# Performance work log

Hardware: AMD Instinct MI355X
Metric: run time of the kernel (lower is better)

Reference implementation:

```python
import jax, jax.numpy as jnp
import numpy as np

# Static config (matches init_kwargs)
B, H, W, C = 8, 80, 60, 512
WS, SHIFT = 10, 5
NH = 16
HD = C // NH  # 32
L = WS * WS  # 100 tokens per window
NW = (H // WS) * (W // WS)  # 48 windows per image
EPS = 1e-5


def _relative_position_index():
    coords = np.stack(np.meshgrid(np.arange(WS), np.arange(WS), indexing='ij'))  # (2,WS,WS)
    flat = coords.reshape(2, -1)  # (2, L)
    rel = flat[:, :, None] - flat[:, None, :]  # (2, L, L)
    rel = rel.transpose(1, 2, 0)  # (L, L, 2)
    rel[:, :, 0] += WS - 1
    rel[:, :, 1] += WS - 1
    rel[:, :, 0] *= 2 * WS - 1
    return rel.sum(-1)  # (L, L) indices into (2*WS-1)^2 table


def _attn_mask():
    # Swin shift mask: label 3x3 regions, tokens in different regions cannot attend.
    img = np.zeros((H, W), dtype=np.float32)
    slices = (slice(0, -WS), slice(-WS, -SHIFT), slice(-SHIFT, None))
    cnt = 0
    for hs in slices:
        for ws_ in slices:
            img[hs, ws_] = cnt
            cnt += 1
    mw = img.reshape(H // WS, WS, W // WS, WS).transpose(0, 2, 1, 3).reshape(NW, L)
    diff = mw[:, None, :] - mw[:, :, None]  # (NW, L, L)
    return np.where(diff != 0, -100.0, 0.0).astype(np.float32)


REL_IDX = jnp.asarray(_relative_position_index())
ATTN_MASK = jnp.asarray(_attn_mask())


def layernorm(x, g, b):
    mu = jnp.mean(x, axis=-1, keepdims=True)
    var = jnp.mean(jnp.square(x - mu), axis=-1, keepdims=True)
    return (x - mu) * jax.lax.rsqrt(var + EPS) * g + b


def setup_inputs() -> dict:
    key = jax.random.key(0)
    ks = jax.random.split(key, 8)
    s = 0.02
    return {
        'hidden_states': jax.random.normal(ks[0], (B, H * W, C), jnp.float32),
        'ln1_g': jnp.ones((C,), jnp.float32),
        'ln1_b': jnp.zeros((C,), jnp.float32),
        'wq': jax.random.normal(ks[1], (C, C), jnp.float32) * s,
        'bq': jnp.zeros((C,), jnp.float32),
        'wk': jax.random.normal(ks[2], (C, C), jnp.float32) * s,
        'bk': jnp.zeros((C,), jnp.float32),
        'wv': jax.random.normal(ks[3], (C, C), jnp.float32) * s,
        'bv': jnp.zeros((C,), jnp.float32),
        'wo': jax.random.normal(ks[4], (C, C), jnp.float32) * s,
        'bo': jnp.zeros((C,), jnp.float32),
        'rel_bias_table': jax.random.normal(ks[5], ((2 * WS - 1) ** 2, NH), jnp.float32) * s,
        'ln2_g': jnp.ones((C,), jnp.float32),
        'ln2_b': jnp.zeros((C,), jnp.float32),
        'w1': jax.random.normal(ks[6], (C, 4 * C), jnp.float32) * s,
        'b1': jnp.zeros((4 * C,), jnp.float32),
        'w2': jax.random.normal(ks[7], (4 * C, C), jnp.float32) * s,
        'b2': jnp.zeros((C,), jnp.float32),
    }


def reference(hidden_states, ln1_g, ln1_b, wq, bq, wk, bk, wv, bv, wo, bo,
              rel_bias_table, ln2_g, ln2_b, w1, b1, w2, b2):
    shortcut = hidden_states  # (B, H*W, C)
    x = layernorm(hidden_states, ln1_g, ln1_b).reshape(B, H, W, C)
    # cyclic shift (H, W divisible by WS -> no padding needed)
    x = jnp.roll(x, (-SHIFT, -SHIFT), axis=(1, 2))
    # window partition -> (B*NW, L, C)
    win = x.reshape(B, H // WS, WS, W // WS, WS, C).transpose(0, 1, 3, 2, 4, 5)
    win = win.reshape(B * NW, L, C)
    # multi-head attention within windows
    q = (win @ wq + bq).reshape(-1, L, NH, HD).transpose(0, 2, 1, 3)
    k = (win @ wk + bk).reshape(-1, L, NH, HD).transpose(0, 2, 1, 3)
    v = (win @ wv + bv).reshape(-1, L, NH, HD).transpose(0, 2, 1, 3)
    scores = jnp.einsum('bhqd,bhkd->bhqk', q, k) / np.sqrt(HD).astype(np.float32)
    bias = rel_bias_table[REL_IDX.reshape(-1)].reshape(L, L, NH).transpose(2, 0, 1)
    scores = scores + bias[None]  # (B*NW, NH, L, L)
    scores = scores.reshape(B, NW, NH, L, L) + ATTN_MASK[None, :, None]
    attn = jax.nn.softmax(scores.reshape(B * NW, NH, L, L), axis=-1)
    ctx = jnp.einsum('bhqk,bhkd->bhqd', attn, v).transpose(0, 2, 1, 3).reshape(B * NW, L, C)
    out = ctx @ wo + bo
    # window reverse + un-shift
    out = out.reshape(B, H // WS, W // WS, WS, WS, C).transpose(0, 1, 3, 2, 4, 5)
    out = out.reshape(B, H, W, C)
    out = jnp.roll(out, (SHIFT, SHIFT), axis=(1, 2)).reshape(B, H * W, C)
    hs = shortcut + out
    # FFN with post-residual layernorm input
    y = layernorm(hs, ln2_g, ln2_b)
    y = jax.nn.gelu(y @ w1 + b1, approximate=False) @ w2 + b2
    return hs + y
```

## Files before the change

kernel.cpp:

```cpp
#include <hip/hip_runtime.h>
#include <math.h>

typedef unsigned short u16;
typedef unsigned int u32;
typedef __bf16 bf16x8 __attribute__((ext_vector_type(8)));
typedef float f32x4 __attribute__((ext_vector_type(4)));

__device__ __forceinline__ float b2f(u16 u) { return __uint_as_float(((u32)u) << 16); }
__device__ __forceinline__ u16 f2b(float f) {
    u32 x = __float_as_uint(f);
    return (u16)((x + 0x7FFFu + ((x >> 16) & 1u)) >> 16);
}
__device__ __forceinline__ void load8f(const float* p, size_t idx, float* o) {
    const float4* q = (const float4*)(p + idx);
    float4 a = q[0], b = q[1];
    o[0]=a.x; o[1]=a.y; o[2]=a.z; o[3]=a.w; o[4]=b.x; o[5]=b.y; o[6]=b.z; o[7]=b.w;
}
__device__ __forceinline__ void gld16(const void* g, void* l) {
    __builtin_amdgcn_global_load_lds(
        (const __attribute__((address_space(1))) u32*)g,
        (__attribute__((address_space(3))) u32*)l, 16, 0, 0);
}

__global__ __launch_bounds__(256) void transpose_k(const float* __restrict__ Win, u16* __restrict__ Wt,
                                                   int Kd, int Nd, float scale) {
    __shared__ u16 tile[32][33];
    int tx = threadIdx.x & 31, ty = threadIdx.x >> 5;
    int k0 = blockIdx.x << 5, n0 = blockIdx.y << 5;
#pragma unroll
    for (int r = 0; r < 4; r++)
        tile[ty + 8 * r][tx] = f2b(Win[(size_t)(k0 + ty + 8 * r) * Nd + (n0 + tx)] * scale);
    __syncthreads();
#pragma unroll
    for (int r = 0; r < 4; r++)
        Wt[(size_t)(n0 + ty + 8 * r) * Kd + (k0 + tx)] = tile[tx][ty + 8 * r];
}

__global__ __launch_bounds__(256) void biascat_k(const float* __restrict__ bq, const float* __restrict__ bk,
                                                 const float* __restrict__ bv, float* __restrict__ o) {
    int i = blockIdx.x * 256 + threadIdx.x;
    float v = (i < 512) ? bq[i] * 0.17677669529663689f : (i < 1024 ? bk[i - 512] : bv[i - 1024]);
    o[i] = v;
}

__global__ __launch_bounds__(256) void ln1win_k(const float* __restrict__ x, const float* __restrict__ g,
                                                const float* __restrict__ bta, u16* __restrict__ win) {
    int wave = threadIdx.x >> 6, lane = threadIdx.x & 63;
    int token = blockIdx.x * 4 + wave;
    int b = token / 4800, rem = token - b * 4800;
    int h = rem / 60, w = rem - h * 60;
    int hr = h + 75; if (hr >= 80) hr -= 80;
    int wr = w + 55; if (wr >= 60) wr -= 60;
    int widx = (hr / 10) * 6 + (wr / 10);
    int l = (hr - (hr / 10) * 10) * 10 + (wr - (wr / 10) * 10);
    size_t dstrow = ((size_t)b * 48 + widx) * 100 + l;
    int c0 = lane * 8;
    float v[8]; load8f(x, (size_t)token * 512 + c0, v);
    float s = 0.f, s2 = 0.f;
#pragma unroll
    for (int e = 0; e < 8; e++) { s += v[e]; s2 += v[e] * v[e]; }
#pragma unroll
    for (int o = 32; o > 0; o >>= 1) { s += __shfl_xor(s, o); s2 += __shfl_xor(s2, o); }
    float mean = s * (1.0f / 512.0f);
    float var = fmaxf(s2 * (1.0f / 512.0f) - mean * mean, 0.0f);
    float rstd = rsqrtf(var + 1e-5f);
    uint4 o4; u16* ou = (u16*)&o4;
#pragma unroll
    for (int e = 0; e < 8; e++)
        ou[e] = f2b((v[e] - mean) * rstd * g[c0 + e] + bta[c0 + e]);
    *(uint4*)(win + dstrow * 512 + c0) = o4;
}

__global__ __launch_bounds__(256) void resid2_k(const float* __restrict__ shortcut, const u16* __restrict__ attn_out,
                                                const float* __restrict__ g, const float* __restrict__ bta,
                                                u16* __restrict__ hs, u16* __restrict__ ln2y) {
    int wave = threadIdx.x >> 6, lane = threadIdx.x & 63;
    int token = blockIdx.x * 4 + wave;
    int b = token / 4800, rem = token - b * 4800;
    int h = rem / 60, w = rem - h * 60;
    int hr = h + 75; if (hr >= 80) hr -= 80;
    int wr = w + 55; if (wr >= 60) wr -= 60;
    int widx = (hr / 10) * 6 + (wr / 10);
    int l = (hr - (hr / 10) * 10) * 10 + (wr - (wr / 10) * 10);
    size_t arow = ((size_t)b * 48 + widx) * 100 + l;
    int c0 = lane * 8;
    float sv[8]; load8f(shortcut, (size_t)token * 512 + c0, sv);
    uint4 da = *(const uint4*)(attn_out + arow * 512 + c0);
    const u16* au = (const u16*)&da;
    float hv[8]; float s = 0.f, s2 = 0.f;
    uint4 oh; u16* ohu = (u16*)&oh;
#pragma unroll
    for (int e = 0; e < 8; e++) {
        hv[e] = sv[e] + b2f(au[e]);
        s += hv[e]; s2 += hv[e] * hv[e];
        ohu[e] = f2b(hv[e]);
    }
    *(uint4*)(hs + (size_t)token * 512 + c0) = oh;
#pragma unroll
    for (int off = 32; off > 0; off >>= 1) { s += __shfl_xor(s, off); s2 += __shfl_xor(s2, off); }
    float mean = s * (1.0f / 512.0f);
    float var = fmaxf(s2 * (1.0f / 512.0f) - mean * mean, 0.0f);
    float rstd = rsqrtf(var + 1e-5f);
    uint4 oy; u16* oyu = (u16*)&oy;
#pragma unroll
    for (int e = 0; e < 8; e++)
        oyu[e] = f2b((hv[e] - mean) * rstd * g[c0 + e] + bta[c0 + e]);
    *(uint4*)(ln2y + (size_t)token * 512 + c0) = oy;
}

template <int EPI, int OF32, int QKV>
__global__ __launch_bounds__(256) void gemm_k(const u16* __restrict__ A, const u16* __restrict__ Bt,
                                              const float* __restrict__ bias, const u16* __restrict__ res,
                                              void* __restrict__ C0, void* __restrict__ C1, void* __restrict__ C2,
                                              int M, int N, int K) {
    __shared__ __align__(16) u16 As[3][128 * 32];
    __shared__ __align__(16) u16 Bs[3][128 * 32];
    int tid = threadIdx.x;
    int wave = tid >> 6, lane = tid & 63;
    int l15 = lane & 15, quad = lane >> 4;
    int lq = lane >> 2, lr = lane & 3;
    int wm = (wave >> 1) * 64, wn = (wave & 1) * 64;

    int gy = gridDim.y;
    int nwg = gridDim.x * gy;
    int lid = blockIdx.x + blockIdx.y * gridDim.x;
    int xcd = lid & 7, loc = lid >> 3;
    int q8 = nwg >> 3, r8 = nwg & 7;
    int wg = (xcd < r8 ? xcd * (q8 + 1) : r8 * (q8 + 1) + (xcd - r8) * q8) + loc;
    int bn = wg % gy, bm = wg / gy;

    f32x4 acc[4][4];
#pragma unroll
    for (int i = 0; i < 4; i++)
#pragma unroll
        for (int j = 0; j < 4; j++) acc[i][j] = (f32x4){0.f, 0.f, 0.f, 0.f};

    const u16* Ab = A + (size_t)(bm * 128) * K;
    const u16* Bb = Bt + (size_t)(bn * 128) * K;

    int T = K >> 5;
    auto STAGE = [&](int b, int t) {
        int kt = t << 5;
#pragma unroll
        for (int h = 0; h < 2; h++) {
            int r = h * 64 + wave * 16 + lq;
            gld16(Ab + (size_t)r * K + kt + lr * 8, &As[b][(h * 64 + wave * 16) * 32]);
            gld16(Bb + (size_t)r * K + kt + lr * 8, &Bs[b][(h * 64 + wave * 16) * 32]);
        }
    };

    STAGE(0, 0);
    STAGE(1, 1);
    for (int t = 0; t < T; t++) {
        int cb = t % 3;
        if (t + 2 < T) STAGE((t + 2) % 3, t + 2);
        if (t + 2 < T)      asm volatile("s_waitcnt vmcnt(8)" ::: "memory");
        else if (t + 1 < T) asm volatile("s_waitcnt vmcnt(4)" ::: "memory");
        else                asm volatile("s_waitcnt vmcnt(0)" ::: "memory");
        __builtin_amdgcn_s_barrier();
        asm volatile("" ::: "memory");
        bf16x8 af[4], bfr[4];
#pragma unroll
        for (int x = 0; x < 4; x++) {
            af[x]  = *(const bf16x8*)(&As[cb][(wm + x * 16 + l15) * 32 + quad * 8]);
            bfr[x] = *(const bf16x8*)(&Bs[cb][(wn + x * 16 + l15) * 32 + quad * 8]);
        }
        asm volatile("s_waitcnt lgkmcnt(0)" ::: "memory");
        __builtin_amdgcn_sched_barrier(0);
        __builtin_amdgcn_s_barrier();
        asm volatile("" ::: "memory");
#pragma unroll
        for (int i = 0; i < 4; i++)
#pragma unroll
            for (int j = 0; j < 4; j++)
                acc[i][j] = __builtin_amdgcn_mfma_f32_16x16x32_bf16(af[i], bfr[j], acc[i][j], 0, 0, 0);
    }

    u16* Cd = (u16*)C0;
    if (QKV) {
        int sel = bn >> 2;
        Cd = (sel == 0) ? (u16*)C0 : (sel == 1) ? (u16*)C1 : (u16*)C2;
    }
#pragma unroll
    for (int i = 0; i < 4; i++) {
        int row0 = bm * 128 + wm + i * 16 + quad * 4;
#pragma unroll
        for (int j = 0; j < 4; j++) {
            int colg = bn * 128 + wn + j * 16 + l15;
            int col = QKV ? (colg & 511) : colg;
            float bv = bias[colg];
#pragma unroll
            for (int rr = 0; rr < 4; rr++) {
                int row = row0 + rr;
                float v = acc[i][j][rr] + bv;
                if (EPI == 1) {
                    float zz = 1.5957691216f * (v + 0.044715f * v * v * v);
                    float t = 1.0f - 2.0f / (__expf(zz) + 1.0f);
                    v = 0.5f * v * (1.0f + t);
                }
                if (EPI == 2) v += b2f(res[(size_t)row * 512 + col]);
                if (OF32) ((float*)Cd)[(size_t)row * N + col] = v;
                else      ((u16*)Cd)[(size_t)row * N + col] = f2b(v);
            }
        }
    }
}

__global__ __launch_bounds__(256) void biasprep_k(const float* __restrict__ table, u16* __restrict__ biasM) {
    int idx = blockIdx.x * 256 + threadIdx.x;
    int k = idx % 112;
    int t = idx / 112;
    int q = t % 100; t /= 100;
    int head = t & 15, wt = t >> 4;
    float v;
    if (k >= 100) {
        v = -1e30f;
    } else {
        int qi = q / 10, qj = q - qi * 10;
        int ki = k / 10, kj = k - ki * 10;
        int rel = (qi - ki) * 19 + (qj - kj) + 180;
        v = table[rel * 16 + head];
        int rq = ((wt & 2) ? (qi < 5 ? 4 : 8) : 0) + ((wt & 1) ? (qj < 5 ? 1 : 2) : 0);
        int rk = ((wt & 2) ? (ki < 5 ? 4 : 8) : 0) + ((wt & 1) ? (kj < 5 ? 1 : 2) : 0);
        if (rq != rk) v -= 100.0f;
    }
    biasM[idx] = f2b(v);
}

__global__ __launch_bounds__(256, 3) void attn_mfma_k(const u16* __restrict__ Q, const u16* __restrict__ Km,
                                                      const u16* __restrict__ V, const u16* __restrict__ biasM,
                                                      u16* __restrict__ ctx) {
    __shared__ __align__(16) u16 lds[4 * 6144];
    int tid = threadIdx.x;
    int wave = tid >> 6, lane = tid & 63;
    int l15 = lane & 15, quad = lane >> 4;
    int bid = blockIdx.x;
    int win = bid >> 2;
    int head = ((bid & 3) << 2) + wave;
    int w48 = win % 48;
    int wh = w48 / 6, ww = w48 - wh * 6;
    int wtype = ((wh == 7) ? 2 : 0) + ((ww == 5) ? 1 : 0);
    size_t base = (size_t)win * 51200 + head * 32;
    u16* Vt = lds + wave * 6144;
    u16* Pl = Vt + 4096;
    const u16* bptr = biasM + (size_t)(wtype * 16 + head) * 11200;

    {
        uint4 z = {0u, 0u, 0u, 0u};
#pragma unroll
        for (int r = 0; r < 2; r++) {
            int c = r * 64 + lane;
            int d = c >> 2, seg = c & 3;
            int k0 = 96 + seg * 8;
            *(uint4*)(Vt + d * 128 + (k0 ^ ((d & 7) << 3))) = z;
        }
        uint2 z2 = {0u, 0u};
        *(uint2*)(Pl + l15 * 128 + ((112 + quad * 4) ^ ((l15 & 7) << 3))) = z2;
    }
#pragma unroll
    for (int r = 0; r < 2; r++) {
        int k = r * 64 + lane;
        if (k < 100) {
            const uint4* vp = (const uint4*)(V + base + (size_t)k * 512);
#pragma unroll
            for (int c = 0; c < 4; c++) {
                uint4 dv = vp[c];
                const u16* e = (const u16*)&dv;
#pragma unroll
                for (int t = 0; t < 8; t++) {
                    int d = c * 8 + t;
                    Vt[d * 128 + (k ^ ((d & 7) << 3))] = e[t];
                }
            }
        }
    }
    bf16x8 kf[7];
#pragma unroll
    for (int i = 0; i < 7; i++) {
        int kr = i * 16 + l15; if (kr > 99) kr = 99;
        kf[i] = *(const bf16x8*)(Km + base + (size_t)kr * 512 + quad * 8);
    }
    bf16x8 vf[2][4];
#pragma unroll
    for (int it = 0; it < 2; it++)
#pragma unroll
        for (int ks = 0; ks < 4; ks++) {
            int D = it * 16 + l15;
            vf[it][ks] = *(const bf16x8*)(Vt + D * 128 + ((ks * 32 + quad * 8) ^ ((D & 7) << 3)));
        }

#pragma unroll 1
    for (int j = 0; j < 7; j++) {
        int q = j * 16 + l15;
        int qc = q > 99 ? 99 : q;
        bf16x8 qf = *(const bf16x8*)(Q + base + (size_t)qc * 512 + quad * 8);
        f32x4 s[7];
#pragma unroll
        for (int i = 0; i < 7; i++) {
            uint2 bb = *(const uint2*)(bptr + (size_t)qc * 112 + i * 16 + quad * 4);
            const u16* be = (const u16*)&bb;
            s[i][0] = b2f(be[0]); s[i][1] = b2f(be[1]);
            s[i][2] = b2f(be[2]); s[i][3] = b2f(be[3]);
        }
#pragma unroll
        for (int i = 0; i < 7; i++)
            s[i] = __builtin_amdgcn_mfma_f32_16x16x32_bf16(kf[i], qf, s[i], 0, 0, 0);
        float m = -1e30f;
#pragma unroll
        for (int i = 0; i < 7; i++)
#pragma unroll
            for (int rr = 0; rr < 4; rr++) m = fmaxf(m, s[i][rr]);
        m = fmaxf(m, __shfl_xor(m, 16));
        m = fmaxf(m, __shfl_xor(m, 32));
        float l = 0.f;
#pragma unroll
        for (int i = 0; i < 7; i++)
#pragma unroll
            for (int rr = 0; rr < 4; rr++) { s[i][rr] = __expf(s[i][rr] - m); l += s[i][rr]; }
        l += __shfl_xor(l, 16);
        l += __shfl_xor(l, 32);
#pragma unroll
        for (int i = 0; i < 7; i++) {
            u32 lo, hi;
            asm("v_cvt_pk_bf16_f32 %0, %1, %2" : "=v"(lo) : "v"(s[i][0]), "v"(s[i][1]));
            asm("v_cvt_pk_bf16_f32 %0, %1, %2" : "=v"(hi) : "v"(s[i][2]), "v"(s[i][3]));
            uint2 w; w.x = lo; w.y = hi;
            *(uint2*)(Pl + l15 * 128 + ((i * 16 + quad * 4) ^ ((l15 & 7) << 3))) = w;
        }
        f32x4 o0 = (f32x4){0.f, 0.f, 0.f, 0.f};
        f32x4 o1 = (f32x4){0.f, 0.f, 0.f, 0.f};
#pragma unroll
        for (int ks = 0; ks < 4; ks++) {
            bf16x8 pf = *(const bf16x8*)(Pl + l15 * 128 + ((ks * 32 + quad * 8) ^ ((l15 & 7) << 3)));
            o0 = __builtin_amdgcn_mfma_f32_16x16x32_bf16(vf[0][ks], pf, o0, 0, 0, 0);
            o1 = __builtin_amdgcn_mfma_f32_16x16x32_bf16(vf[1][ks], pf, o1, 0, 0, 0);
        }
        float inv = 1.0f / l;
        if (q < 100) {
            u16* cp = ctx + base + (size_t)q * 512;
            {
                float a0 = o0[0]*inv, a1 = o0[1]*inv, a2 = o0[2]*inv, a3 = o0[3]*inv;
                u32 lo, hi;
                asm("v_cvt_pk_bf16_f32 %0, %1, %2" : "=v"(lo) : "v"(a0), "v"(a1));
                asm("v_cvt_pk_bf16_f32 %0, %1, %2" : "=v"(hi) : "v"(a2), "v"(a3));
                uint2 w; w.x = lo; w.y = hi;
                *(uint2*)(cp + quad * 4) = w;
            }
            {
                float a0 = o1[0]*inv, a1 = o1[1]*inv, a2 = o1[2]*inv, a3 = o1[3]*inv;
                u32 lo, hi;
                asm("v_cvt_pk_bf16_f32 %0, %1, %2" : "=v"(lo) : "v"(a0), "v"(a1));
                asm("v_cvt_pk_bf16_f32 %0, %1, %2" : "=v"(hi) : "v"(a2), "v"(a3));
                uint2 w; w.x = lo; w.y = hi;
                *(uint2*)(cp + 16 + quad * 4) = w;
            }
        }
    }
}

extern "C" void kernel_launch(void* const* d_in, const int* in_sizes, int n_in,
                              void* d_out, int out_size, void* d_ws, size_t ws_size,
                              hipStream_t stream) {
    const float* hidden = (const float*)d_in[0];
    const float* ln1_g  = (const float*)d_in[1];
    const float* ln1_b  = (const float*)d_in[2];
    const float* wq = (const float*)d_in[3];  const float* bq = (const float*)d_in[4];
    const float* wk = (const float*)d_in[5];  const float* bk = (const float*)d_in[6];
    const float* wv = (const float*)d_in[7];  const float* bv = (const float*)d_in[8];
    const float* wo = (const float*)d_in[9];  const float* bo = (const float*)d_in[10];
    const float* rel = (const float*)d_in[11];
    const float* ln2_g = (const float*)d_in[12];
    const float* ln2_b = (const float*)d_in[13];
    const float* w1 = (const float*)d_in[14]; const float* b1 = (const float*)d_in[15];
    const float* w2 = (const float*)d_in[16]; const float* b2 = (const float*)d_in[17];

    const size_t NTC = 38400ull * 512;
    u16* ws = (u16*)d_ws;
    u16* R0 = ws;
    u16* R1 = ws + NTC;
    u16* Rh = ws + 2 * NTC;
    u16* wqt = ws + 3 * NTC;
    u16* wkt = wqt + 512 * 512;
    u16* wvt = wkt + 512 * 512;
    u16* wot = wvt + 512 * 512;
    u16* w1t = wot + 512 * 512;
    u16* w2t = w1t + 1048576;
    float* qkvb = (float*)(w2t + 1048576);
    u16* dlo = (u16*)d_out;
    u16* biasM = dlo + NTC;
    float* outp = (float*)d_out;

    const float SC = 0.17677669529663689f;

    transpose_k<<<dim3(16, 16), 256, 0, stream>>>(wq, wqt, 512, 512, SC);
    transpose_k<<<dim3(16, 16), 256, 0, stream>>>(wk, wkt, 512, 512, 1.0f);
    transpose_k<<<dim3(16, 16), 256, 0, stream>>>(wv, wvt, 512, 512, 1.0f);
    transpose_k<<<dim3(16, 16), 256, 0, stream>>>(wo, wot, 512, 512, 1.0f);
    transpose_k<<<dim3(16, 64), 256, 0, stream>>>(w1, w1t, 512, 2048, 1.0f);
    transpose_k<<<dim3(64, 16), 256, 0, stream>>>(w2, w2t, 2048, 512, 1.0f);
    biascat_k<<<6, 256, 0, stream>>>(bq, bk, bv, qkvb);
    biasprep_k<<<2800, 256, 0, stream>>>(rel, biasM);

    ln1win_k<<<9600, 256, 0, stream>>>(hidden, ln1_g, ln1_b, R0 );

    gemm_k<0, 0, 1><<<dim3(300, 12), 256, 0, stream>>>(R0, wqt, qkvb, nullptr,
                                                       R1 , Rh , dlo , 38400, 512, 512);

    attn_mfma_k<<<1536, 256, 0, stream>>>(R1, Rh, dlo, biasM, R0 );

    gemm_k<0, 0, 0><<<dim3(300, 4), 256, 0, stream>>>(R0, wot, bo, nullptr,
                                                      R1 , nullptr, nullptr, 38400, 512, 512);

    resid2_k<<<9600, 256, 0, stream>>>(hidden, R1, ln2_g, ln2_b, Rh , dlo );

    for (int mc = 1; mc >= 0; mc--) {
        size_t roff = (size_t)mc * 19200 * 512;
        gemm_k<1, 0, 0><<<dim3(150, 16), 256, 0, stream>>>(dlo + roff, w1t, b1, nullptr,
                                                           R0 , nullptr, nullptr, 19200, 2048, 512);
        gemm_k<2, 1, 0><<<dim3(150, 4), 256, 0, stream>>>(R0, w2t, b2, Rh + roff,
                                                          outp + roff, nullptr, nullptr, 19200, 512, 2048);
    }
}
```

Before: 724.9 us.

## Enlarge GEMM tiles to 256x256x64 with 8 waves, swizzled LDS and split-phase prefetch

Rewrites the bf16 MFMA GEMM to use 256x256 output tiles with K-step 64, 512 threads (8 waves, each computing 128x64), and double-buffered LDS with an XOR swizzle to avoid bank conflicts. Global-to-LDS prefetch of the next tile is interleaved between MFMA phases, and s_setprio raises priority around the MFMA bursts. The aim is higher arithmetic intensity per LDS/global byte and better latency hiding. In exchange it uses more registers and LDS (128 KB) and launches a quarter as many workgroups, which can hurt occupancy or tail balance on the 38400x512 GEMMs.

Result: slower. 752.3 us (+3.8%).

```diff
diff --git a/kernel.cpp b/kernel.cpp
--- a/kernel.cpp
+++ b/kernel.cpp
@@ -109,17 +109,16 @@
 }
 
 template <int EPI, int OF32, int QKV>
-__global__ __launch_bounds__(256) void gemm_k(const u16* __restrict__ A, const u16* __restrict__ Bt,
-                                              const float* __restrict__ bias, const u16* __restrict__ res,
-                                              void* __restrict__ C0, void* __restrict__ C1, void* __restrict__ C2,
-                                              int M, int N, int K) {
-    __shared__ __align__(16) u16 As[3][128 * 32];
-    __shared__ __align__(16) u16 Bs[3][128 * 32];
+__global__ __launch_bounds__(512, 2) void gemm_k(const u16* __restrict__ A, const u16* __restrict__ Bt,
+                                                 const float* __restrict__ bias, const u16* __restrict__ res,
+                                                 void* __restrict__ C0, void* __restrict__ C1, void* __restrict__ C2,
+                                                 int M, int N, int K) {
+    __shared__ __align__(16) u16 As[2][256 * 64];
+    __shared__ __align__(16) u16 Bs[2][256 * 64];
     int tid = threadIdx.x;
     int wave = tid >> 6, lane = tid & 63;
     int l15 = lane & 15, quad = lane >> 4;
-    int lq = lane >> 2, lr = lane & 3;
-    int wm = (wave >> 1) * 64, wn = (wave & 1) * 64;
+    int wr = wave >> 2, wc = wave & 3;
 
     int gy = gridDim.y;
     int nwg = gridDim.x * gy;
@@ -129,74 +128,115 @@
     int wg = (xcd < r8 ? xcd * (q8 + 1) : r8 * (q8 + 1) + (xcd - r8) * q8) + loc;
     int bn = wg % gy, bm = wg / gy;
 
-    f32x4 acc[4][4];
-#pragma unroll
-    for (int i = 0; i < 4; i++)
+    f32x4 acc[8][4];
+#pragma unroll
+    for (int i = 0; i < 8; i++)
 #pragma unroll
         for (int j = 0; j < 4; j++) acc[i][j] = (f32x4){0.f, 0.f, 0.f, 0.f};
 
-    const u16* Ab = A + (size_t)(bm * 128) * K;
-    const u16* Bb = Bt + (size_t)(bn * 128) * K;
-
-    int T = K >> 5;
-    auto STAGE = [&](int b, int t) {
-        int kt = t << 5;
-#pragma unroll
-        for (int h = 0; h < 2; h++) {
-            int r = h * 64 + wave * 16 + lq;
-            gld16(Ab + (size_t)r * K + kt + lr * 8, &As[b][(h * 64 + wave * 16) * 32]);
-            gld16(Bb + (size_t)r * K + kt + lr * 8, &Bs[b][(h * 64 + wave * 16) * 32]);
-        }
+    const u16* Ab = A + (size_t)(bm * 256) * K;
+    const u16* Bb = Bt + (size_t)(bn * 256) * K;
+
+    int lrow = lane >> 3;
+    int cg = (lane & 7) ^ lrow;
+    size_t gOff = (size_t)(wave * 8 + lrow) * K + cg * 8;
+    int e = l15 & 7;
+    int xk0 = (quad ^ e) * 8;
+    int xk1 = xk0 ^ 32;
+    int aRow = (wr * 128 + l15) * 64;
+    int bRow = (wc * 64 + l15) * 64;
+
+    auto STAGE_A = [&](int b, int kt, int i) {
+        gld16(Ab + (size_t)(i * 64) * K + kt + gOff, &As[b][(i * 64 + wave * 8) * 64]);
     };
-
-    STAGE(0, 0);
-    STAGE(1, 1);
+    auto STAGE_B = [&](int b, int kt, int j) {
+        gld16(Bb + (size_t)(j * 64) * K + kt + gOff, &Bs[b][(j * 64 + wave * 8) * 64]);
+    };
+
+#define MM16(MH)                                                                     \
+    do {                                                                             \
+        __builtin_amdgcn_s_setprio(1);                                               \
+        _Pragma("unroll") for (int i_ = 0; i_ < 4; i_++)                             \
+            _Pragma("unroll") for (int n_ = 0; n_ < 4; n_++)                         \
+                acc[(MH) * 4 + i_][n_] = __builtin_amdgcn_mfma_f32_16x16x32_bf16(    \
+                    a_[i_], b_[n_], acc[(MH) * 4 + i_][n_], 0, 0, 0);                \
+        __builtin_amdgcn_s_setprio(0);                                               \
+    } while (0)
+
+    int T = K >> 6;
+    STAGE_B(0, 0, 0); STAGE_B(0, 0, 1);
+    STAGE_B(0, 0, 2); STAGE_B(0, 0, 3);
+    STAGE_A(0, 0, 0); STAGE_A(0, 0, 2);
+    STAGE_A(0, 0, 1); STAGE_A(0, 0, 3);
+
+#pragma unroll 1
     for (int t = 0; t < T; t++) {
-        int cb = t % 3;
-        if (t + 2 < T) STAGE((t + 2) % 3, t + 2);
-        if (t + 2 < T)      asm volatile("s_waitcnt vmcnt(8)" ::: "memory");
-        else if (t + 1 < T) asm volatile("s_waitcnt vmcnt(4)" ::: "memory");
-        else                asm volatile("s_waitcnt vmcnt(0)" ::: "memory");
+        int cur = t & 1, nxt = cur ^ 1;
+        int ktn = (t + 1) << 6;
+        bool pf = (t + 1 < T);
+        bf16x8 a_[4], b_[4];
+        if (pf) {
+            STAGE_B(nxt, ktn, 0); STAGE_B(nxt, ktn, 1);
+            asm volatile("s_waitcnt vmcnt(4)" ::: "memory");
+        } else {
+            asm volatile("s_waitcnt vmcnt(2)" ::: "memory");
+        }
         __builtin_amdgcn_s_barrier();
         asm volatile("" ::: "memory");
-        bf16x8 af[4], bfr[4];
-#pragma unroll
-        for (int x = 0; x < 4; x++) {
-            af[x]  = *(const bf16x8*)(&As[cb][(wm + x * 16 + l15) * 32 + quad * 8]);
-            bfr[x] = *(const bf16x8*)(&Bs[cb][(wn + x * 16 + l15) * 32 + quad * 8]);
-        }
+#pragma unroll
+        for (int n = 0; n < 4; n++) b_[n] = *(const bf16x8*)(&Bs[cur][bRow + n * 1024 + xk0]);
+#pragma unroll
+        for (int i = 0; i < 4; i++) a_[i] = *(const bf16x8*)(&As[cur][aRow + i * 1024 + xk0]);
+        MM16(0);
+        if (pf) {
+            STAGE_B(nxt, ktn, 2); STAGE_B(nxt, ktn, 3);
+            asm volatile("s_waitcnt vmcnt(4)" ::: "memory");
+        } else {
+            asm volatile("s_waitcnt vmcnt(0)" ::: "memory");
+        }
+        __builtin_amdgcn_s_barrier();
+        asm volatile("" ::: "memory");
+#pragma unroll
+        for (int i = 0; i < 4; i++) a_[i] = *(const bf16x8*)(&As[cur][aRow + (4 + i) * 1024 + xk0]);
+        MM16(1);
+        if (pf) { STAGE_A(nxt, ktn, 0); STAGE_A(nxt, ktn, 2); }
+#pragma unroll
+        for (int n = 0; n < 4; n++) b_[n] = *(const bf16x8*)(&Bs[cur][bRow + n * 1024 + xk1]);
+#pragma unroll
+        for (int i = 0; i < 4; i++) a_[i] = *(const bf16x8*)(&As[cur][aRow + i * 1024 + xk1]);
+        MM16(0);
+        if (pf) { STAGE_A(nxt, ktn, 1); STAGE_A(nxt, ktn, 3); }
+#pragma unroll
+        for (int i = 0; i < 4; i++) a_[i] = *(const bf16x8*)(&As[cur][aRow + (4 + i) * 1024 + xk1]);
         asm volatile("s_waitcnt lgkmcnt(0)" ::: "memory");
         __builtin_amdgcn_sched_barrier(0);
         __builtin_amdgcn_s_barrier();
         asm volatile("" ::: "memory");
-#pragma unroll
-        for (int i = 0; i < 4; i++)
-#pragma unroll
-            for (int j = 0; j < 4; j++)
-                acc[i][j] = __builtin_amdgcn_mfma_f32_16x16x32_bf16(af[i], bfr[j], acc[i][j], 0, 0, 0);
-    }
+        MM16(1);
+    }
+#undef MM16
 
     u16* Cd = (u16*)C0;
     if (QKV) {
-        int sel = bn >> 2;
+        int sel = bn >> 1;
         Cd = (sel == 0) ? (u16*)C0 : (sel == 1) ? (u16*)C1 : (u16*)C2;
     }
 #pragma unroll
-    for (int i = 0; i < 4; i++) {
-        int row0 = bm * 128 + wm + i * 16 + quad * 4;
-#pragma unroll
-        for (int j = 0; j < 4; j++) {
-            int colg = bn * 128 + wn + j * 16 + l15;
+    for (int m = 0; m < 8; m++) {
+        int row0 = bm * 256 + wr * 128 + m * 16 + quad * 4;
+#pragma unroll
+        for (int n = 0; n < 4; n++) {
+            int colg = bn * 256 + wc * 64 + n * 16 + l15;
             int col = QKV ? (colg & 511) : colg;
             float bv = bias[colg];
 #pragma unroll
             for (int rr = 0; rr < 4; rr++) {
                 int row = row0 + rr;
-                float v = acc[i][j][rr] + bv;
+                float v = acc[m][n][rr] + bv;
                 if (EPI == 1) {
                     float zz = 1.5957691216f * (v + 0.044715f * v * v * v);
-                    float t = 1.0f - 2.0f / (__expf(zz) + 1.0f);
-                    v = 0.5f * v * (1.0f + t);
+                    float tt = 1.0f - 2.0f / (__expf(zz) + 1.0f);
+                    v = 0.5f * v * (1.0f + tt);
                 }
                 if (EPI == 2) v += b2f(res[(size_t)row * 512 + col]);
                 if (OF32) ((float*)Cd)[(size_t)row * N + col] = v;
@@ -403,21 +443,21 @@
 
     ln1win_k<<<9600, 256, 0, stream>>>(hidden, ln1_g, ln1_b, R0 );
 
-    gemm_k<0, 0, 1><<<dim3(300, 12), 256, 0, stream>>>(R0, wqt, qkvb, nullptr,
-                                                       R1 , Rh , dlo , 38400, 512, 512);
+    gemm_k<0, 0, 1><<<dim3(150, 6), 512, 0, stream>>>(R0, wqt, qkvb, nullptr,
+                                                      R1 , Rh , dlo , 38400, 512, 512);
 
     attn_mfma_k<<<1536, 256, 0, stream>>>(R1, Rh, dlo, biasM, R0 );
 
-    gemm_k<0, 0, 0><<<dim3(300, 4), 256, 0, stream>>>(R0, wot, bo, nullptr,
+    gemm_k<0, 0, 0><<<dim3(150, 2), 512, 0, stream>>>(R0, wot, bo, nullptr,
                                                       R1 , nullptr, nullptr, 38400, 512, 512);
 
     resid2_k<<<9600, 256, 0, stream>>>(hidden, R1, ln2_g, ln2_b, Rh , dlo );
 
     for (int mc = 1; mc >= 0; mc--) {
         size_t roff = (size_t)mc * 19200 * 512;
-        gemm_k<1, 0, 0><<<dim3(150, 16), 256, 0, stream>>>(dlo + roff, w1t, b1, nullptr,
-                                                           R0 , nullptr, nullptr, 19200, 2048, 512);
-        gemm_k<2, 1, 0><<<dim3(150, 4), 256, 0, stream>>>(R0, w2t, b2, Rh + roff,
-                                                          outp + roff, nullptr, nullptr, 19200, 512, 2048);
-    }
-}
+        gemm_k<1, 0, 0><<<dim3(75, 8), 512, 0, stream>>>(dlo + roff, w1t, b1, nullptr,
+                                                         R0 , nullptr, nullptr, 19200, 2048, 512);
+        gemm_k<2, 1, 0><<<dim3(75, 2), 512, 0, stream>>>(R0, w2t, b2, Rh + roff,
+                                                         outp + roff, nullptr, nullptr, 19200, 512, 2048);
+    }
+}
```
